# Kernel tuning notes

Hardware: AMD Instinct MI355X
Metric: run time of the kernel (lower is better)

## Reference

```python
import jax, jax.numpy as jnp
import numpy as np

HEADS = 8
EPS = 1e-5


def setup_inputs() -> dict:
    key = jax.random.key(0)
    ks = jax.random.split(key, 8)
    B, S, D = 4, 2048, 512
    inputs = jax.random.normal(ks[0], (B, S, D), dtype=jnp.float32)
    mask = jnp.ones((B, S), dtype=jnp.int32)
    sc = 1.0 / np.sqrt(D)
    # torch Linear weights stored transposed as [in, out] for x @ W
    W_qkv = jax.random.uniform(ks[1], (D, 3 * D), jnp.float32, -sc, sc)
    b_qkv = jax.random.uniform(ks[2], (3 * D,), jnp.float32, -sc, sc)
    W_o = jax.random.uniform(ks[3], (D, D), jnp.float32, -sc, sc)
    b_o = jax.random.uniform(ks[4], (D,), jnp.float32, -sc, sc)
    gamma = jnp.ones((D,), jnp.float32)
    beta = jnp.zeros((D,), jnp.float32)
    return {"inputs": inputs, "mask": mask, "W_qkv": W_qkv, "b_qkv": b_qkv,
            "W_o": W_o, "b_o": b_o, "gamma": gamma, "beta": beta}


def reference(inputs, mask, W_qkv, b_qkv, W_o, b_o, gamma, beta):
    B, S, D = inputs.shape
    H = HEADS
    dh = D // H
    t = inputs @ W_qkv + b_qkv                      # [B,S,3D]
    q, k, v = jnp.split(t, 3, axis=-1)
    # [B,S,D] -> [B,H,S,dh]
    q = q.reshape(B, S, H, dh).transpose(0, 2, 1, 3)
    k = k.reshape(B, S, H, dh).transpose(0, 2, 1, 3)
    v = v.reshape(B, S, H, dh).transpose(0, 2, 1, 3)
    # unscaled dot-product attention (is_scaled=False in the source)
    scores = jnp.einsum('bhqd,bhkd->bhqk', q, k)    # [B,H,S,S]
    key_mask = (mask > 0)[:, None, None, :]         # broadcast over heads & query rows
    scores = jnp.where(key_mask, scores, -jnp.inf)
    attn = jax.nn.softmax(scores, axis=-1)
    att = jnp.einsum('bhqk,bhkd->bhqd', attn, v)    # [B,H,S,dh]
    att = att.transpose(0, 2, 1, 3).reshape(B, S, D)
    out = att @ W_o + b_o
    x = out + att                                    # residual
    mu = jnp.mean(x, axis=-1, keepdims=True)
    var = jnp.mean(jnp.square(x - mu), axis=-1, keepdims=True)
    return (x - mu) / jnp.sqrt(var + EPS) * gamma + beta
```

## Files before the change

kernel.cpp:

```cpp
#include <hip/hip_runtime.h>
#include <cstdint>

#define S_LEN 2048
#define D_MODEL 512
#define H_NUM 8
#define DH 64
#define LOG2E 1.4426950408889634f

typedef __attribute__((ext_vector_type(8))) short bf16x8;
typedef __attribute__((ext_vector_type(8))) unsigned short u16x8;
typedef __attribute__((ext_vector_type(4))) float f32x4;

__device__ inline unsigned short f2bf(float x) {
    unsigned int u = __builtin_bit_cast(unsigned int, x);
    u += 0x7fffu + ((u >> 16) & 1u);
    return (unsigned short)(u >> 16);
}
__device__ inline float bf2f(unsigned short u) {
    return __builtin_bit_cast(float, (unsigned int)u << 16);
}
__device__ inline unsigned pack_bf2(float a, float b) {
    unsigned ua = __builtin_bit_cast(unsigned, a) + 0x8000u;
    unsigned ub = __builtin_bit_cast(unsigned, b) + 0x8000u;
    return __builtin_amdgcn_perm(ub, ua, 0x07060302);
}

__device__ inline void async_ld16(const unsigned short* g, unsigned short* l) {
    __builtin_amdgcn_global_load_lds(
        (const __attribute__((address_space(1))) unsigned int*)(const unsigned int*)g,
        (__attribute__((address_space(3))) unsigned int*)(unsigned int*)l,
        16, 0, 0);
}

__global__ __launch_bounds__(256) void prep(
    const float* __restrict__ X, const float* __restrict__ Wqkv,
    const float* __restrict__ Wo,
    unsigned short* __restrict__ Xb, unsigned short* __restrict__ WqkvT,
    unsigned short* __restrict__ WoT)
{
    __shared__ float tile[32][36];
    const int blk = blockIdx.x;
    const int tid = threadIdx.x;
    if (blk < 1024) {
        const int base = blk * 4096 + tid * 16;
        #pragma unroll
        for (int i = 0; i < 4; ++i) {
            float4 v = *(const float4*)(X + base + i * 4);
            ushort4 o;
            o.x = f2bf(v.x); o.y = f2bf(v.y); o.z = f2bf(v.z); o.w = f2bf(v.w);
            *(ushort4*)(Xb + base + i * 4) = o;
        }
        return;
    }
    const float* src; unsigned short* dst; int N, t;
    if (blk < 1792) { src = Wqkv; dst = WqkvT; N = 1536; t = blk - 1024; }
    else            { src = Wo;   dst = WoT;   N = 512;  t = blk - 1792; }
    const int tnx = N / 32;
    const int bx = t % tnx;
    const int by = t / tnx;
    const int row = tid >> 3;
    const int c4  = (tid & 7) * 4;
    *(float4*)&tile[row][c4] = *(const float4*)(src + (size_t)(by * 32 + row) * N + bx * 32 + c4);
    __syncthreads();
    ushort4 o;
    o.x = f2bf(tile[c4 + 0][row]);
    o.y = f2bf(tile[c4 + 1][row]);
    o.z = f2bf(tile[c4 + 2][row]);
    o.w = f2bf(tile[c4 + 3][row]);
    *(ushort4*)(dst + (size_t)(bx * 32 + row) * 512 + by * 32 + c4) = o;
}

__global__ __launch_bounds__(256) void qkv_mfma(
    const unsigned short* __restrict__ Xb, const unsigned short* __restrict__ WT,
    const float* __restrict__ bias,
    unsigned short* __restrict__ Q, unsigned short* __restrict__ K,
    unsigned short* __restrict__ Vt)
{
    __shared__ unsigned short sA[128 * 64];
    __shared__ unsigned short sB[128 * 64];
    const int tid  = threadIdx.x;
    const int w    = tid >> 6;
    const int lane = tid & 63;
    const int l16  = lane & 15;
    const int quad = lane >> 4;
    const int wm = w >> 1, wn = w & 1;
    const int n0 = blockIdx.x * 128;
    const int m0 = blockIdx.y * 128;

    const unsigned short* gA[4]; const unsigned short* gB[4];
    unsigned short *lA[4], *lB[4];
    #pragma unroll
    for (int j = 0; j < 4; ++j) {
        const int ci = tid + j * 256;
        const int row = ci >> 3;
        const int col = ((ci & 7) ^ (row & 7)) * 8;
        gA[j] = Xb + (size_t)(m0 + row) * 512 + col;
        gB[j] = WT + (size_t)(n0 + row) * 512 + col;
        lA[j] = sA + ci * 8 - lane * 8;
        lB[j] = sB + ci * 8 - lane * 8;
    }

    f32x4 acc[4][4] = {};
    for (int k0 = 0; k0 < 512; k0 += 64) {
        __syncthreads();
        #pragma unroll
        for (int j = 0; j < 4; ++j) {
            async_ld16(gA[j] + k0, lA[j]);
            async_ld16(gB[j] + k0, lB[j]);
        }
        __syncthreads();
        bf16x8 a[4][2], bfr[4][2];
        #pragma unroll
        for (int mi = 0; mi < 4; ++mi) {
            const int row = wm * 64 + mi * 16 + l16;
            a[mi][0] = *(const bf16x8*)&sA[row * 64 + ((quad       ^ (row & 7)) * 8)];
            a[mi][1] = *(const bf16x8*)&sA[row * 64 + (((4 + quad) ^ (row & 7)) * 8)];
        }
        #pragma unroll
        for (int ni = 0; ni < 4; ++ni) {
            const int row = wn * 64 + ni * 16 + l16;
            bfr[ni][0] = *(const bf16x8*)&sB[row * 64 + ((quad       ^ (row & 7)) * 8)];
            bfr[ni][1] = *(const bf16x8*)&sB[row * 64 + (((4 + quad) ^ (row & 7)) * 8)];
        }
        #pragma unroll
        for (int mi = 0; mi < 4; ++mi)
            #pragma unroll
            for (int ni = 0; ni < 4; ++ni) {
                acc[mi][ni] = __builtin_amdgcn_mfma_f32_16x16x32_bf16(a[mi][0], bfr[ni][0], acc[mi][ni], 0, 0, 0);
                acc[mi][ni] = __builtin_amdgcn_mfma_f32_16x16x32_bf16(a[mi][1], bfr[ni][1], acc[mi][ni], 0, 0, 0);
            }
    }

    const int which = n0 >> 9;
    const int h = ((n0 & 511) >> 6) + wn;
    const int b = m0 >> 11;
    const int sbase = (m0 & 2047) + wm * 64;
    float bv[4];
    #pragma unroll
    for (int ni = 0; ni < 4; ++ni) bv[ni] = bias[n0 + wn * 64 + ni * 16 + l16];
    if (which == 2) {
        #pragma unroll
        for (int ni = 0; ni < 4; ++ni) {
            const int dh = ni * 16 + l16;
            unsigned short* vp = Vt + ((size_t)(b * H_NUM + h) * DH + dh) * S_LEN;
            #pragma unroll
            for (int mi = 0; mi < 4; ++mi) {
                const int s0 = sbase + mi * 16 + quad * 4;
                ushort4 o;
                o.x = f2bf(acc[mi][ni][0] + bv[ni]);
                o.y = f2bf(acc[mi][ni][1] + bv[ni]);
                o.z = f2bf(acc[mi][ni][2] + bv[ni]);
                o.w = f2bf(acc[mi][ni][3] + bv[ni]);
                *(ushort4*)(vp + s0) = o;
            }
        }
    } else {
        const float qs = (which == 0) ? LOG2E : 1.0f;
        unsigned short* dst = (which == 0) ? Q : K;
        dst += (size_t)(b * H_NUM + h) * S_LEN * DH;
        #pragma unroll
        for (int mi = 0; mi < 4; ++mi)
            #pragma unroll
            for (int r = 0; r < 4; ++r) {
                const int s = sbase + mi * 16 + quad * 4 + r;
                #pragma unroll
                for (int ni = 0; ni < 4; ++ni)
                    dst[(size_t)s * DH + ni * 16 + l16] = f2bf((acc[mi][ni][r] + bv[ni]) * qs);
            }
    }
}

__global__ __launch_bounds__(256) void attn_mfma(
    const unsigned short* __restrict__ Q, const unsigned short* __restrict__ K,
    const unsigned short* __restrict__ Vt, const int* __restrict__ mask,
    unsigned short* __restrict__ att)
{
    __shared__ unsigned short sK[2][64 * 64];
    __shared__ unsigned short sVt[2][64 * 64];
    __shared__ unsigned short sP[4][32][72];
    __shared__ float smbt[2][64];

    const int tid  = threadIdx.x;
    const int w    = tid >> 6;
    const int lane = tid & 63;
    const int l16  = lane & 15;
    const int quad = lane >> 4;
    const int qt = blockIdx.x;
    const int bh = blockIdx.y;
    const int b  = bh >> 3;
    const int h  = bh & 7;
    const size_t kbase = (size_t)bh * S_LEN * DH;
    const size_t vbase = (size_t)bh * DH * S_LEN;

    bf16x8 qf[2][2];
    {
        const unsigned short* qp = Q + kbase + (size_t)(qt * 128 + w * 16 + l16) * DH + quad * 8;
        qf[0][0] = *(const bf16x8*)qp;
        qf[0][1] = *(const bf16x8*)(qp + 32);
        qf[1][0] = *(const bf16x8*)(qp + 64 * DH);
        qf[1][1] = *(const bf16x8*)(qp + 64 * DH + 32);
    }

    const int ci0 = w * 128 + lane;
    const int ci1 = ci0 + 64;
    const int r0_ = ci0 >> 3, c0_ = ((ci0 & 7) ^ (r0_ & 7)) * 8;
    const int r1_ = ci1 >> 3, c1_ = ((ci1 & 7) ^ (r1_ & 7)) * 8;
    const int kOff0 = r0_ * 64 + c0_;
    const int kOff1 = r1_ * 64 + c1_;
    const int vOff0 = r0_ * S_LEN + c0_;
    const int vOff1 = r1_ * S_LEN + c1_;
    const int lds0 = ci0 * 8 - lane * 8;
    const int lds1 = ci1 * 8 - lane * 8;

    bf16x8 vones;
    #pragma unroll
    for (int j = 0; j < 8; ++j) vones[j] = (short)0x3F80;

    f32x4 O[2][4] = {};
    f32x4 Ol[2] = {};

    {
        const unsigned short* gK = K  + kbase;
        const unsigned short* gV = Vt + vbase;
        async_ld16(gK + kOff0, sK[0] + lds0);
        async_ld16(gK + kOff1, sK[0] + lds1);
        async_ld16(gV + vOff0, sVt[0] + lds0);
        async_ld16(gV + vOff1, sVt[0] + lds1);
        if (tid < 64) smbt[0][tid] = mask[b * S_LEN + tid] ? 0.f : -1e30f;
    }

    for (int kt = 0; kt < 32; ++kt) {
        const int cur = kt & 1, nxt = cur ^ 1;
        __syncthreads();
        if (kt + 1 < 32) {
            const unsigned short* gK = K  + kbase + (size_t)(kt + 1) * 64 * DH;
            const unsigned short* gV = Vt + vbase + (kt + 1) * 64;
            async_ld16(gK + kOff0, sK[nxt] + lds0);
            async_ld16(gK + kOff1, sK[nxt] + lds1);
            async_ld16(gV + vOff0, sVt[nxt] + lds0);
            async_ld16(gV + vOff1, sVt[nxt] + lds1);
            if (tid < 64) smbt[nxt][tid] = mask[b * S_LEN + (kt + 1) * 64 + tid] ? 0.f : -1e30f;
        }
        const unsigned short* sKc  = sK[cur];
        const unsigned short* sVtc = sVt[cur];

        bf16x8 kb[4][2];
        #pragma unroll
        for (int nb = 0; nb < 4; ++nb) {
            const int row = nb * 16 + l16;
            const int x = row & 7;
            kb[nb][0] = *(const bf16x8*)&sKc[row * 64 + ((quad       ^ x) * 8)];
            kb[nb][1] = *(const bf16x8*)&sKc[row * 64 + (((4 + quad) ^ x) * 8)];
        }
        float4 mb[4];
        #pragma unroll
        for (int nb = 0; nb < 4; ++nb)
            mb[nb] = *(const float4*)&smbt[cur][nb * 16 + quad * 4];

        #pragma unroll
        for (int t = 0; t < 2; ++t) {
            f32x4 c[4] = {{0,0,0,0},{0,0,0,0},{0,0,0,0},{0,0,0,0}};
            #pragma unroll
            for (int nb = 0; nb < 4; ++nb) {
                c[nb] = __builtin_amdgcn_mfma_f32_16x16x32_bf16(kb[nb][0], qf[t][0], c[nb], 0, 0, 0);
                c[nb] = __builtin_amdgcn_mfma_f32_16x16x32_bf16(kb[nb][1], qf[t][1], c[nb], 0, 0, 0);
            }
            #pragma unroll
            for (int nb = 0; nb < 4; ++nb) {
                const float p0 = __builtin_amdgcn_exp2f(c[nb][0] + mb[nb].x);
                const float p1 = __builtin_amdgcn_exp2f(c[nb][1] + mb[nb].y);
                const float p2 = __builtin_amdgcn_exp2f(c[nb][2] + mb[nb].z);
                const float p3 = __builtin_amdgcn_exp2f(c[nb][3] + mb[nb].w);
                uint2 pk;
                pk.x = pack_bf2(p0, p1);
                pk.y = pack_bf2(p2, p3);
                *(uint2*)&sP[w][t * 16 + l16][nb * 16 + quad * 4] = pk;
            }
        }

        bf16x8 vb[4][2];
        #pragma unroll
        for (int db = 0; db < 4; ++db) {
            const int row = db * 16 + l16;
            const int x = row & 7;
            vb[db][0] = *(const bf16x8*)&sVtc[row * 64 + ((quad       ^ x) * 8)];
            vb[db][1] = *(const bf16x8*)&sVtc[row * 64 + (((4 + quad) ^ x) * 8)];
        }
        #pragma unroll
        for (int t = 0; t < 2; ++t) {
            const bf16x8 pa0 = *(const bf16x8*)&sP[w][t * 16 + l16][quad * 8];
            const bf16x8 pa1 = *(const bf16x8*)&sP[w][t * 16 + l16][quad * 8 + 32];
            #pragma unroll
            for (int db = 0; db < 4; ++db) {
                O[t][db] = __builtin_amdgcn_mfma_f32_16x16x32_bf16(pa0, vb[db][0], O[t][db], 0, 0, 0);
                O[t][db] = __builtin_amdgcn_mfma_f32_16x16x32_bf16(pa1, vb[db][1], O[t][db], 0, 0, 0);
            }
            Ol[t] = __builtin_amdgcn_mfma_f32_16x16x32_bf16(pa0, vones, Ol[t], 0, 0, 0);
            Ol[t] = __builtin_amdgcn_mfma_f32_16x16x32_bf16(pa1, vones, Ol[t], 0, 0, 0);
        }
    }

    #pragma unroll
    for (int t = 0; t < 2; ++t) {
        #pragma unroll
        for (int r = 0; r < 4; ++r) {
            const float invr = 1.0f / Ol[t][r];
            const size_t grow = (size_t)b * S_LEN + qt * 128 + t * 64 + w * 16 + quad * 4 + r;
            unsigned short* op = att + grow * D_MODEL + h * DH + l16;
            op[0]  = f2bf(O[t][0][r] * invr);
            op[16] = f2bf(O[t][1][r] * invr);
            op[32] = f2bf(O[t][2][r] * invr);
            op[48] = f2bf(O[t][3][r] * invr);
        }
    }
}

__global__ __launch_bounds__(256) void proj_mfma(
    const unsigned short* __restrict__ attb, const unsigned short* __restrict__ WoT,
    const float* __restrict__ bo, float* __restrict__ xbuf)
{
    __shared__ unsigned short sA[128 * 64];
    __shared__ unsigned short sB[64 * 64];
    const int tid  = threadIdx.x;
    const int w    = tid >> 6;
    const int lane = tid & 63;
    const int l16  = lane & 15;
    const int quad = lane >> 4;
    const int wm = w >> 1, wn = w & 1;
    const int n0 = blockIdx.x * 64;
    const int m0 = blockIdx.y * 128;

    const unsigned short* gA[4]; unsigned short* lA[4];
    const unsigned short* gB[2]; unsigned short* lB[2];
    #pragma unroll
    for (int j = 0; j < 4; ++j) {
        const int ci = tid + j * 256;
        const int row = ci >> 3;
        const int col = ((ci & 7) ^ (row & 7)) * 8;
        gA[j] = attb + (size_t)(m0 + row) * 512 + col;
        lA[j] = sA + ci * 8 - lane * 8;
    }
    #pragma unroll
    for (int j = 0; j < 2; ++j) {
        const int ci = tid + j * 256;
        const int row = ci >> 3;
        const int col = ((ci & 7) ^ (row & 7)) * 8;
        gB[j] = WoT + (size_t)(n0 + row) * 512 + col;
        lB[j] = sB + ci * 8 - lane * 8;
    }

    f32x4 acc[4][2] = {};
    for (int k0 = 0; k0 < 512; k0 += 64) {
        __syncthreads();
        #pragma unroll
        for (int j = 0; j < 4; ++j) async_ld16(gA[j] + k0, lA[j]);
        #pragma unroll
        for (int j = 0; j < 2; ++j) async_ld16(gB[j] + k0, lB[j]);
        __syncthreads();
        bf16x8 a[4][2], bfr[2][2];
        #pragma unroll
        for (int mi = 0; mi < 4; ++mi) {
            const int row = wm * 64 + mi * 16 + l16;
            a[mi][0] = *(const bf16x8*)&sA[row * 64 + ((quad       ^ (row & 7)) * 8)];
            a[mi][1] = *(const bf16x8*)&sA[row * 64 + (((4 + quad) ^ (row & 7)) * 8)];
        }
        #pragma unroll
        for (int ni = 0; ni < 2; ++ni) {
            const int row = wn * 32 + ni * 16 + l16;
            bfr[ni][0] = *(const bf16x8*)&sB[row * 64 + ((quad       ^ (row & 7)) * 8)];
            bfr[ni][1] = *(const bf16x8*)&sB[row * 64 + (((4 + quad) ^ (row & 7)) * 8)];
        }
        #pragma unroll
        for (int mi = 0; mi < 4; ++mi)
            #pragma unroll
            for (int ni = 0; ni < 2; ++ni) {
                acc[mi][ni] = __builtin_amdgcn_mfma_f32_16x16x32_bf16(a[mi][0], bfr[ni][0], acc[mi][ni], 0, 0, 0);
                acc[mi][ni] = __builtin_amdgcn_mfma_f32_16x16x32_bf16(a[mi][1], bfr[ni][1], acc[mi][ni], 0, 0, 0);
            }
    }

    #pragma unroll
    for (int ni = 0; ni < 2; ++ni) {
        const int n = n0 + wn * 32 + ni * 16 + l16;
        const float bv = bo[n];
        #pragma unroll
        for (int mi = 0; mi < 4; ++mi) {
            #pragma unroll
            for (int r = 0; r < 4; ++r) {
                const int m = m0 + wm * 64 + mi * 16 + quad * 4 + r;
                const float resid = bf2f(attb[(size_t)m * 512 + n]);
                xbuf[(size_t)m * 512 + n] = acc[mi][ni][r] + bv + resid;
            }
        }
    }
}

__global__ __launch_bounds__(256) void ln_kernel(
    const float* __restrict__ xbuf, const float* __restrict__ gamma,
    const float* __restrict__ beta, float* __restrict__ out)
{
    const int tid = threadIdx.x;
    const int w = tid >> 6, lane = tid & 63;
    const size_t row = (size_t)blockIdx.x * 4 + w;
    const float* xp = xbuf + row * 512 + lane * 8;
    float4 v0 = *(const float4*)xp;
    float4 v1 = *(const float4*)(xp + 4);
    float s  = v0.x + v0.y + v0.z + v0.w + v1.x + v1.y + v1.z + v1.w;
    float sq = v0.x*v0.x + v0.y*v0.y + v0.z*v0.z + v0.w*v0.w
             + v1.x*v1.x + v1.y*v1.y + v1.z*v1.z + v1.w*v1.w;
    #pragma unroll
    for (int off = 1; off < 64; off <<= 1) {
        s  += __shfl_xor(s, off, 64);
        sq += __shfl_xor(sq, off, 64);
    }
    const float mu = s * (1.0f / 512.0f);
    const float var = sq * (1.0f / 512.0f) - mu * mu;
    const float rs = rsqrtf(var + 1e-5f);
    float4 g0 = *(const float4*)(gamma + lane * 8);
    float4 g1 = *(const float4*)(gamma + lane * 8 + 4);
    float4 b0 = *(const float4*)(beta + lane * 8);
    float4 b1 = *(const float4*)(beta + lane * 8 + 4);
    float4 o0, o1;
    o0.x = (v0.x - mu) * rs * g0.x + b0.x;
    o0.y = (v0.y - mu) * rs * g0.y + b0.y;
    o0.z = (v0.z - mu) * rs * g0.z + b0.z;
    o0.w = (v0.w - mu) * rs * g0.w + b0.w;
    o1.x = (v1.x - mu) * rs * g1.x + b1.x;
    o1.y = (v1.y - mu) * rs * g1.y + b1.y;
    o1.z = (v1.z - mu) * rs * g1.z + b1.z;
    o1.w = (v1.w - mu) * rs * g1.w + b1.w;
    float* op = out + row * 512 + lane * 8;
    *(float4*)op = o0;
    *(float4*)(op + 4) = o1;
}

extern "C" void kernel_launch(void* const* d_in, const int* in_sizes, int n_in,
                              void* d_out, int out_size, void* d_ws, size_t ws_size,
                              hipStream_t stream)
{
    (void)in_sizes; (void)n_in; (void)out_size; (void)ws_size;
    const float* X    = (const float*)d_in[0];
    const int*   mask = (const int*)d_in[1];
    const float* Wqkv = (const float*)d_in[2];
    const float* bqkv = (const float*)d_in[3];
    const float* Wo   = (const float*)d_in[4];
    const float* bo   = (const float*)d_in[5];
    const float* gamma= (const float*)d_in[6];
    const float* beta = (const float*)d_in[7];
    float* out = (float*)d_out;

    const size_t NE = (size_t)4 * S_LEN * D_MODEL;
    unsigned short* ws16 = (unsigned short*)d_ws;
    unsigned short* Xb     = ws16;
    unsigned short* WqkvT  = Xb + NE;
    unsigned short* WoT    = WqkvT + 786432;
    unsigned short* Q      = WoT + 262144;
    unsigned short* K      = Q + NE;
    unsigned short* Vt     = K + NE;
    unsigned short* attb   = Vt + NE;
    float* xbuf = (float*)(attb + NE);

    prep<<<dim3(2048), 256, 0, stream>>>(X, Wqkv, Wo, Xb, WqkvT, WoT);
    qkv_mfma<<<dim3(12, 64), 256, 0, stream>>>(Xb, WqkvT, bqkv, Q, K, Vt);
    attn_mfma<<<dim3(16, 32), 256, 0, stream>>>(Q, K, Vt, mask, attb);
    proj_mfma<<<dim3(8, 64), 256, 0, stream>>>(attb, WoT, bo, xbuf);
    ln_kernel<<<dim3(2048), 256, 0, stream>>>(xbuf, gamma, beta, out);
}
```

Baseline: 181.9 us.

## Split attention key tiles across wave pairs and reduce partial outputs in LDS

Each block's four waves now form two query groups of 64 rows by two key halves of 32 columns, instead of each wave owning 32 query rows over all 64 keys. Each wave loads only half the K tile and one V k-slice per iteration. The partial O and row sums are combined through shared memory at the end. A launch bound of 2 blocks per CU is added, and shared memory is packed into a single byte buffer that is reused for the reduction. This trades a larger per-wave accumulator and an end-of-kernel LDS reduction for smaller per-iteration LDS reads and a tighter score-to-PV dependency per 16-row tile.

Result: no change. 180.9 us (-0.6%).

```diff
diff --git a/kernel.cpp b/kernel.cpp
--- a/kernel.cpp
+++ b/kernel.cpp
@@ -170,35 +170,42 @@
     }
 }
 
-__global__ __launch_bounds__(256) void attn_mfma(
+__global__ __launch_bounds__(256, 2) void attn_mfma(
     const unsigned short* __restrict__ Q, const unsigned short* __restrict__ K,
     const unsigned short* __restrict__ Vt, const int* __restrict__ mask,
     unsigned short* __restrict__ att)
 {
-    __shared__ unsigned short sK[2][64 * 64];
-    __shared__ unsigned short sVt[2][64 * 64];
-    __shared__ unsigned short sP[4][32][72];
-    __shared__ float smbt[2][64];
+    __shared__ __align__(16) char smem[38400];
+    unsigned short* sK  = (unsigned short*)smem;
+    unsigned short* sVt = (unsigned short*)(smem + 16384);
+    unsigned short* sP  = (unsigned short*)(smem + 32768);
+    float* smbt = (float*)(smem + 37888);
+    float* red  = (float*)smem;
+    float* lred = (float*)(smem + 34816);
 
     const int tid  = threadIdx.x;
     const int w    = tid >> 6;
     const int lane = tid & 63;
     const int l16  = lane & 15;
     const int quad = lane >> 4;
+    const int qg = w >> 1;
+    const int kg = w & 1;
     const int qt = blockIdx.x;
     const int bh = blockIdx.y;
     const int b  = bh >> 3;
     const int h  = bh & 7;
     const size_t kbase = (size_t)bh * S_LEN * DH;
     const size_t vbase = (size_t)bh * DH * S_LEN;
-
-    bf16x8 qf[2][2];
+    unsigned short* sPw = sP + w * 640;
+
+    bf16x8 qf[4][2];
     {
-        const unsigned short* qp = Q + kbase + (size_t)(qt * 128 + w * 16 + l16) * DH + quad * 8;
-        qf[0][0] = *(const bf16x8*)qp;
-        qf[0][1] = *(const bf16x8*)(qp + 32);
-        qf[1][0] = *(const bf16x8*)(qp + 64 * DH);
-        qf[1][1] = *(const bf16x8*)(qp + 64 * DH + 32);
+        const unsigned short* qp = Q + kbase + (size_t)(qt * 128 + qg * 64 + l16) * DH + quad * 8;
+        #pragma unroll
+        for (int t = 0; t < 4; ++t) {
+            qf[t][0] = *(const bf16x8*)(qp + t * 16 * DH);
+            qf[t][1] = *(const bf16x8*)(qp + t * 16 * DH + 32);
+        }
     }
 
     const int ci0 = w * 128 + lane;
@@ -216,17 +223,17 @@
     #pragma unroll
     for (int j = 0; j < 8; ++j) vones[j] = (short)0x3F80;
 
-    f32x4 O[2][4] = {};
-    f32x4 Ol[2] = {};
+    f32x4 O[4][4] = {};
+    f32x4 Ol[4] = {};
 
     {
         const unsigned short* gK = K  + kbase;
         const unsigned short* gV = Vt + vbase;
-        async_ld16(gK + kOff0, sK[0] + lds0);
-        async_ld16(gK + kOff1, sK[0] + lds1);
-        async_ld16(gV + vOff0, sVt[0] + lds0);
-        async_ld16(gV + vOff1, sVt[0] + lds1);
-        if (tid < 64) smbt[0][tid] = mask[b * S_LEN + tid] ? 0.f : -1e30f;
+        async_ld16(gK + kOff0, sK + lds0);
+        async_ld16(gK + kOff1, sK + lds1);
+        async_ld16(gV + vOff0, sVt + lds0);
+        async_ld16(gV + vOff1, sVt + lds1);
+        if (tid < 64) smbt[tid] = mask[b * S_LEN + tid] ? 0.f : -1e30f;
     }
 
     for (int kt = 0; kt < 32; ++kt) {
@@ -235,82 +242,100 @@
         if (kt + 1 < 32) {
             const unsigned short* gK = K  + kbase + (size_t)(kt + 1) * 64 * DH;
             const unsigned short* gV = Vt + vbase + (kt + 1) * 64;
-            async_ld16(gK + kOff0, sK[nxt] + lds0);
-            async_ld16(gK + kOff1, sK[nxt] + lds1);
-            async_ld16(gV + vOff0, sVt[nxt] + lds0);
-            async_ld16(gV + vOff1, sVt[nxt] + lds1);
-            if (tid < 64) smbt[nxt][tid] = mask[b * S_LEN + (kt + 1) * 64 + tid] ? 0.f : -1e30f;
-        }
-        const unsigned short* sKc  = sK[cur];
-        const unsigned short* sVtc = sVt[cur];
-
-        bf16x8 kb[4][2];
-        #pragma unroll
-        for (int nb = 0; nb < 4; ++nb) {
-            const int row = nb * 16 + l16;
+            async_ld16(gK + kOff0, sK + nxt * 4096 + lds0);
+            async_ld16(gK + kOff1, sK + nxt * 4096 + lds1);
+            async_ld16(gV + vOff0, sVt + nxt * 4096 + lds0);
+            async_ld16(gV + vOff1, sVt + nxt * 4096 + lds1);
+            if (tid < 64) smbt[nxt * 64 + tid] = mask[b * S_LEN + (kt + 1) * 64 + tid] ? 0.f : -1e30f;
+        }
+        const unsigned short* sKc = sK  + cur * 4096;
+        const unsigned short* sVc = sVt + cur * 4096;
+
+        bf16x8 kb[2][2];
+        #pragma unroll
+        for (int kpb = 0; kpb < 2; ++kpb) {
+            const int row = kg * 32 + kpb * 16 + l16;
             const int x = row & 7;
-            kb[nb][0] = *(const bf16x8*)&sKc[row * 64 + ((quad       ^ x) * 8)];
-            kb[nb][1] = *(const bf16x8*)&sKc[row * 64 + (((4 + quad) ^ x) * 8)];
-        }
-        float4 mb[4];
-        #pragma unroll
-        for (int nb = 0; nb < 4; ++nb)
-            mb[nb] = *(const float4*)&smbt[cur][nb * 16 + quad * 4];
-
-        #pragma unroll
-        for (int t = 0; t < 2; ++t) {
-            f32x4 c[4] = {{0,0,0,0},{0,0,0,0},{0,0,0,0},{0,0,0,0}};
-            #pragma unroll
-            for (int nb = 0; nb < 4; ++nb) {
-                c[nb] = __builtin_amdgcn_mfma_f32_16x16x32_bf16(kb[nb][0], qf[t][0], c[nb], 0, 0, 0);
-                c[nb] = __builtin_amdgcn_mfma_f32_16x16x32_bf16(kb[nb][1], qf[t][1], c[nb], 0, 0, 0);
-            }
-            #pragma unroll
-            for (int nb = 0; nb < 4; ++nb) {
-                const float p0 = __builtin_amdgcn_exp2f(c[nb][0] + mb[nb].x);
-                const float p1 = __builtin_amdgcn_exp2f(c[nb][1] + mb[nb].y);
-                const float p2 = __builtin_amdgcn_exp2f(c[nb][2] + mb[nb].z);
-                const float p3 = __builtin_amdgcn_exp2f(c[nb][3] + mb[nb].w);
-                uint2 pk;
-                pk.x = pack_bf2(p0, p1);
-                pk.y = pack_bf2(p2, p3);
-                *(uint2*)&sP[w][t * 16 + l16][nb * 16 + quad * 4] = pk;
-            }
-        }
-
-        bf16x8 vb[4][2];
+            kb[kpb][0] = *(const bf16x8*)&sKc[row * 64 + ((quad       ^ x) * 8)];
+            kb[kpb][1] = *(const bf16x8*)&sKc[row * 64 + (((4 + quad) ^ x) * 8)];
+        }
+        float4 mb[2];
+        #pragma unroll
+        for (int kpb = 0; kpb < 2; ++kpb)
+            mb[kpb] = *(const float4*)&smbt[cur * 64 + kg * 32 + kpb * 16 + quad * 4];
+
+        bf16x8 vb[4];
         #pragma unroll
         for (int db = 0; db < 4; ++db) {
             const int row = db * 16 + l16;
             const int x = row & 7;
-            vb[db][0] = *(const bf16x8*)&sVtc[row * 64 + ((quad       ^ x) * 8)];
-            vb[db][1] = *(const bf16x8*)&sVtc[row * 64 + (((4 + quad) ^ x) * 8)];
-        }
-        #pragma unroll
-        for (int t = 0; t < 2; ++t) {
-            const bf16x8 pa0 = *(const bf16x8*)&sP[w][t * 16 + l16][quad * 8];
-            const bf16x8 pa1 = *(const bf16x8*)&sP[w][t * 16 + l16][quad * 8 + 32];
+            vb[db] = *(const bf16x8*)&sVc[row * 64 + (((4 * kg + quad) ^ x) * 8)];
+        }
+
+        #pragma unroll
+        for (int t = 0; t < 4; ++t) {
+            f32x4 c0 = {0,0,0,0}, c1 = {0,0,0,0};
+            c0 = __builtin_amdgcn_mfma_f32_16x16x32_bf16(kb[0][0], qf[t][0], c0, 0, 0, 0);
+            c0 = __builtin_amdgcn_mfma_f32_16x16x32_bf16(kb[0][1], qf[t][1], c0, 0, 0, 0);
+            c1 = __builtin_amdgcn_mfma_f32_16x16x32_bf16(kb[1][0], qf[t][0], c1, 0, 0, 0);
+            c1 = __builtin_amdgcn_mfma_f32_16x16x32_bf16(kb[1][1], qf[t][1], c1, 0, 0, 0);
+
+            const float p00 = __builtin_amdgcn_exp2f(c0[0] + mb[0].x);
+            const float p01 = __builtin_amdgcn_exp2f(c0[1] + mb[0].y);
+            const float p02 = __builtin_amdgcn_exp2f(c0[2] + mb[0].z);
+            const float p03 = __builtin_amdgcn_exp2f(c0[3] + mb[0].w);
+            const float p10 = __builtin_amdgcn_exp2f(c1[0] + mb[1].x);
+            const float p11 = __builtin_amdgcn_exp2f(c1[1] + mb[1].y);
+            const float p12 = __builtin_amdgcn_exp2f(c1[2] + mb[1].z);
+            const float p13 = __builtin_amdgcn_exp2f(c1[3] + mb[1].w);
+            uint2 pk0, pk1;
+            pk0.x = pack_bf2(p00, p01); pk0.y = pack_bf2(p02, p03);
+            pk1.x = pack_bf2(p10, p11); pk1.y = pack_bf2(p12, p13);
+            *(uint2*)&sPw[l16 * 40 + quad * 4]      = pk0;
+            *(uint2*)&sPw[l16 * 40 + 16 + quad * 4] = pk1;
+
+            const bf16x8 pa = *(const bf16x8*)&sPw[l16 * 40 + quad * 8];
+            #pragma unroll
+            for (int db = 0; db < 4; ++db)
+                O[t][db] = __builtin_amdgcn_mfma_f32_16x16x32_bf16(pa, vb[db], O[t][db], 0, 0, 0);
+            Ol[t] = __builtin_amdgcn_mfma_f32_16x16x32_bf16(pa, vones, Ol[t], 0, 0, 0);
+        }
+    }
+
+    __syncthreads();
+    if (kg == 1) {
+        #pragma unroll
+        for (int t = 0; t < 4; ++t) {
             #pragma unroll
             for (int db = 0; db < 4; ++db) {
-                O[t][db] = __builtin_amdgcn_mfma_f32_16x16x32_bf16(pa0, vb[db][0], O[t][db], 0, 0, 0);
-                O[t][db] = __builtin_amdgcn_mfma_f32_16x16x32_bf16(pa1, vb[db][1], O[t][db], 0, 0, 0);
-            }
-            Ol[t] = __builtin_amdgcn_mfma_f32_16x16x32_bf16(pa0, vones, Ol[t], 0, 0, 0);
-            Ol[t] = __builtin_amdgcn_mfma_f32_16x16x32_bf16(pa1, vones, Ol[t], 0, 0, 0);
-        }
-    }
-
-    #pragma unroll
-    for (int t = 0; t < 2; ++t) {
-        #pragma unroll
-        for (int r = 0; r < 4; ++r) {
-            const float invr = 1.0f / Ol[t][r];
-            const size_t grow = (size_t)b * S_LEN + qt * 128 + t * 64 + w * 16 + quad * 4 + r;
-            unsigned short* op = att + grow * D_MODEL + h * DH + l16;
-            op[0]  = f2bf(O[t][0][r] * invr);
-            op[16] = f2bf(O[t][1][r] * invr);
-            op[32] = f2bf(O[t][2][r] * invr);
-            op[48] = f2bf(O[t][3][r] * invr);
+                #pragma unroll
+                for (int r = 0; r < 4; ++r)
+                    red[(size_t)(qg * 64 + t * 16 + quad * 4 + r) * 68 + db * 16 + l16] = O[t][db][r];
+            }
+            if (l16 == 0) {
+                #pragma unroll
+                for (int r = 0; r < 4; ++r)
+                    lred[qg * 64 + t * 16 + quad * 4 + r] = Ol[t][r];
+            }
+        }
+    }
+    __syncthreads();
+    if (kg == 0) {
+        #pragma unroll
+        for (int t = 0; t < 4; ++t) {
+            #pragma unroll
+            for (int r = 0; r < 4; ++r) {
+                const int lrow = qg * 64 + t * 16 + quad * 4 + r;
+                const float l = Ol[t][r] + lred[lrow];
+                const float invr = 1.0f / l;
+                const size_t grow = (size_t)b * S_LEN + qt * 128 + lrow;
+                unsigned short* op = att + grow * D_MODEL + h * DH + l16;
+                #pragma unroll
+                for (int db = 0; db < 4; ++db) {
+                    const float v = (O[t][db][r] + red[(size_t)lrow * 68 + db * 16 + l16]) * invr;
+                    op[db * 16] = f2bf(v);
+                }
+            }
         }
     }
 }
```
